# Kernel optimization log

Hardware: AMD Instinct MI355X
Metric: run time of the kernel (lower is better)

The kernel has to match this reference:

```python
import jax, jax.numpy as jnp
import numpy as np

B, S, H = 32, 512, 256
MAX_MEL = 2000  # init kwarg max_mel_len
DUR_MAX = 8


def setup_inputs() -> dict:
    key = jax.random.key(0)
    k1, k2 = jax.random.split(key)
    x = jax.random.normal(k1, (B, S, H), dtype=jnp.float32)
    duration = jax.random.randint(k2, (B, S), 0, DUR_MAX, dtype=jnp.int32)
    return {"x": x, "duration": duration, "max_len": MAX_MEL}


def reference(x, duration, max_len):
    # x: [B, S, H]; duration: [B, S] int; max_len unused (kept for API parity).
    batch, seq_len, hidden = x.shape
    max_mel = MAX_MEL

    cumsum = jnp.cumsum(duration, axis=1)            # [B, S]
    pos = jnp.arange(max_mel, dtype=cumsum.dtype)    # [T]

    # Original builds mask = (pos < cumsum[:, :, None]) and takes argmax over S
    # (index of first True), falling back to seq_len-1 when no True, then clamps.
    # That is exactly searchsorted(cumsum, pos, side='right') clipped to S-1:
    # first j with cumsum[j] > pos; returns S (-> clipped to S-1) when pos >= total.
    idx = jax.vmap(lambda c: jnp.searchsorted(c, pos, side='right'))(cumsum)  # [B, T]
    idx = jnp.clip(idx, 0, seq_len - 1)

    output = jnp.take_along_axis(x, idx[:, :, None], axis=1)  # [B, T, H]

    mel_len = jnp.clip(jnp.sum(duration, axis=1), None, max_mel).astype(jnp.int32)  # [B]
    return output, mel_len
```

## Files before the change

kernel.cpp:

```cpp
#include <hip/hip_runtime.h>

constexpr int B_ = 32;
constexpr int S_ = 512;
constexpr int H_ = 256;
constexpr int T_ = 2000;
constexpr int F4 = H_ / 4;
constexpr int RPS = 16;
constexpr int N_SCAT = S_ / RPS;
constexpr int TAIL_CHUNK = 125;
constexpr int N_TAIL = (T_ + TAIL_CHUNK - 1) / TAIL_CHUNK;

typedef float f32x4 __attribute__((ext_vector_type(4)));

__global__ __launch_bounds__(256) void lenreg_scatter_kernel(
    const f32x4* __restrict__ x,
    const int* __restrict__ dur,
    const int* __restrict__ max_len_p,
    f32x4* __restrict__ out,
    float* __restrict__ mel_len_out)
{
    const int b = blockIdx.y;
    const int role = blockIdx.x;
    const int tid = threadIdx.x;
    const int lane = tid & 63;
    const int wave = tid >> 6;

    __shared__ int s_cum[S_];
    __shared__ int s_wsum[4];

    const f32x4* __restrict__ x_b = x + (size_t)b * S_ * F4;
    f32x4* __restrict__ out_b = out + (size_t)b * T_ * F4;

    f32x4 v[RPS / 4];
    int s0 = 0;
    if (role < N_SCAT) {
        s0 = role * RPS + wave * (RPS / 4);
#pragma unroll
        for (int i = 0; i < RPS / 4; ++i)
            v[i] = x_b[(size_t)(s0 + i) * F4 + lane];
    } else {
        v[0] = x_b[(size_t)(S_ - 1) * F4 + lane];
    }

    const int2 d2 = ((const int2*)(dur + b * S_))[tid];
    const int pair = d2.x + d2.y;
    int scan = pair;
#pragma unroll
    for (int off = 1; off < 64; off <<= 1) {
        const int y = __shfl_up(scan, off);
        if (lane >= off) scan += y;
    }
    if (lane == 63) s_wsum[wave] = scan;
    __syncthreads();
    int wprefix = 0;
#pragma unroll
    for (int w = 0; w < 4; ++w) wprefix += (w < wave) ? s_wsum[w] : 0;
    const int excl = wprefix + scan - pair;
    s_cum[2 * tid]     = excl + d2.x;
    s_cum[2 * tid + 1] = excl + pair;
    __syncthreads();

    const int total = s_cum[S_ - 1];

    if (role < N_SCAT) {
#pragma unroll
        for (int i = 0; i < RPS / 4; ++i) {
            const int s = s0 + i;
            const int lo = s ? s_cum[s - 1] : 0;
            int hi = s_cum[s]; if (hi > T_) hi = T_;
            for (int t = lo; t < hi; ++t)
                out_b[(size_t)t * F4 + lane] = v[i];
        }
    } else {
        const int j = role - N_SCAT;
        if (j == 0 && tid == 0) {
            const int ml = max_len_p[0];
            mel_len_out[b] = (float)(total < ml ? total : ml);
        }
        int t_begin = j * TAIL_CHUNK;
        int t_end = t_begin + TAIL_CHUNK; if (t_end > T_) t_end = T_;
        if (t_begin < total) t_begin = total;
        for (int t = t_begin + wave; t < t_end; t += 4)
            out_b[(size_t)t * F4 + lane] = v[0];
    }
}

extern "C" void kernel_launch(void* const* d_in, const int* in_sizes, int n_in,
                              void* d_out, int out_size, void* d_ws, size_t ws_size,
                              hipStream_t stream) {
    const f32x4* x = (const f32x4*)d_in[0];
    const int* duration = (const int*)d_in[1];
    const int* max_len_p = (const int*)d_in[2];

    float* out = (float*)d_out;
    float* mel_len_out = out + (size_t)B_ * T_ * H_;

    dim3 grid(N_SCAT + N_TAIL, B_);
    lenreg_scatter_kernel<<<grid, 256, 0, stream>>>(
        x, duration, max_len_p, (f32x4*)out, mel_len_out);
}
```

Baseline: 88.24 us.

## Stage rows in LDS and interleave output rows across waves; merge tail into scatter blocks

Each block stores its 16 source rows in shared memory, and all four waves take turns over the block's whole output range, using a shared-memory pointer walk to find each source row. This replaces the old per-wave serial loops, which were imbalanced. The separate tail-fill blocks are removed, and the tail rows past the total duration are striped across all scatter blocks. In exchange it adds shared-memory traffic and an extra read of the last row in every block, and the grid now has fewer blocks.

```diff
diff --git a/kernel.cpp b/kernel.cpp
--- a/kernel.cpp
+++ b/kernel.cpp
@@ -7,8 +7,6 @@
 constexpr int F4 = H_ / 4;
 constexpr int RPS = 16;
 constexpr int N_SCAT = S_ / RPS;
-constexpr int TAIL_CHUNK = 125;
-constexpr int N_TAIL = (T_ + TAIL_CHUNK - 1) / TAIL_CHUNK;
 
 typedef float f32x4 __attribute__((ext_vector_type(4)));
 
@@ -27,20 +25,18 @@
 
     __shared__ int s_cum[S_];
     __shared__ int s_wsum[4];
+    __shared__ f32x4 s_rows[RPS][F4];
 
     const f32x4* __restrict__ x_b = x + (size_t)b * S_ * F4;
     f32x4* __restrict__ out_b = out + (size_t)b * T_ * F4;
 
+    const int s0 = role * RPS;
+    const int sw = s0 + wave * (RPS / 4);
     f32x4 v[RPS / 4];
-    int s0 = 0;
-    if (role < N_SCAT) {
-        s0 = role * RPS + wave * (RPS / 4);
 #pragma unroll
-        for (int i = 0; i < RPS / 4; ++i)
-            v[i] = x_b[(size_t)(s0 + i) * F4 + lane];
-    } else {
-        v[0] = x_b[(size_t)(S_ - 1) * F4 + lane];
-    }
+    for (int i = 0; i < RPS / 4; ++i)
+        v[i] = x_b[(size_t)(sw + i) * F4 + lane];
+    const f32x4 vtail = x_b[(size_t)(S_ - 1) * F4 + lane];
 
     const int2 d2 = ((const int2*)(dur + b * S_))[tid];
     const int pair = d2.x + d2.y;
@@ -58,30 +54,29 @@
     const int excl = wprefix + scan - pair;
     s_cum[2 * tid]     = excl + d2.x;
     s_cum[2 * tid + 1] = excl + pair;
+
+#pragma unroll
+    for (int i = 0; i < RPS / 4; ++i)
+        s_rows[wave * (RPS / 4) + i][lane] = v[i];
     __syncthreads();
 
     const int total = s_cum[S_ - 1];
 
-    if (role < N_SCAT) {
-#pragma unroll
-        for (int i = 0; i < RPS / 4; ++i) {
-            const int s = s0 + i;
-            const int lo = s ? s_cum[s - 1] : 0;
-            int hi = s_cum[s]; if (hi > T_) hi = T_;
-            for (int t = lo; t < hi; ++t)
-                out_b[(size_t)t * F4 + lane] = v[i];
-        }
-    } else {
-        const int j = role - N_SCAT;
-        if (j == 0 && tid == 0) {
-            const int ml = max_len_p[0];
-            mel_len_out[b] = (float)(total < ml ? total : ml);
-        }
-        int t_begin = j * TAIL_CHUNK;
-        int t_end = t_begin + TAIL_CHUNK; if (t_end > T_) t_end = T_;
-        if (t_begin < total) t_begin = total;
-        for (int t = t_begin + wave; t < t_end; t += 4)
-            out_b[(size_t)t * F4 + lane] = v[0];
+    const int lo = s0 ? s_cum[s0 - 1] : 0;
+    int hi = s_cum[s0 + RPS - 1];
+    if (hi > T_) hi = T_;
+    int sp = 0;
+    for (int t = lo + wave; t < hi; t += 4) {
+        while (s_cum[s0 + sp] <= t) ++sp;
+        out_b[(size_t)t * F4 + lane] = s_rows[sp][lane];
+    }
+
+    for (int t = total + role * 4 + wave; t < T_; t += 4 * N_SCAT)
+        out_b[(size_t)t * F4 + lane] = vtail;
+
+    if (role == 0 && tid == 0) {
+        const int ml = max_len_p[0];
+        mel_len_out[b] = (float)(total < ml ? total : ml);
     }
 }
 
@@ -95,7 +90,7 @@
     float* out = (float*)d_out;
     float* mel_len_out = out + (size_t)B_ * T_ * H_;
 
-    dim3 grid(N_SCAT + N_TAIL, B_);
+    dim3 grid(N_SCAT, B_);
     lenreg_scatter_kernel<<<grid, 256, 0, stream>>>(
         x, duration, max_len_p, (f32x4*)out, mel_len_out);
 }
```

After: 84.65 us. 4.1% less time.
